# Kernel optimization log

Measured on AMD Instinct MI355X. Metric: run time of the kernel, lower is better.

Reference implementation:

```python
import jax, jax.numpy as jnp
import numpy as np

H = 8        # n_heads (== n_kv_heads)
D = 128      # head_dim
WINDOW = 16  # sliding window (left); causal => right window = 0
EPS = 1e-6   # qk_norm_eps


def rms_norm(x, w, eps=EPS):
    # RMSNorm over last dim with learnable scale
    ms = jnp.mean(jnp.square(x), axis=-1, keepdims=True)
    return x * jax.lax.rsqrt(ms + eps) * w


def setup_inputs() -> dict:
    key = jax.random.key(0)
    ks = jax.random.split(key, 5)
    B, S, dim = 4, 2048, 1024
    scale = 1.0 / np.sqrt(dim)
    return {
        "x": jax.random.normal(ks[0], (B, S, dim), jnp.float32),
        "wq": jax.random.normal(ks[1], (dim, dim), jnp.float32) * scale,
        "wk": jax.random.normal(ks[2], (dim, dim), jnp.float32) * scale,
        "wv": jax.random.normal(ks[3], (dim, dim), jnp.float32) * scale,
        "wo": jax.random.normal(ks[4], (dim, dim), jnp.float32) * scale,
        "q_norm_w": jnp.ones((dim,), jnp.float32),
        "k_norm_w": jnp.ones((dim,), jnp.float32),
    }


def reference(x, wq, wk, wv, wo, q_norm_w, k_norm_w):
    B, S, dim = x.shape
    # projections (torch Linear: x @ W.T)
    xq = rms_norm(x @ wq.T, q_norm_w)
    xk = rms_norm(x @ wk.T, k_norm_w)
    xv = x @ wv.T
    q = xq.reshape(B, S, H, D)
    k = xk.reshape(B, S, H, D)
    v = xv.reshape(B, S, H, D)

    # ALiBi slopes for 8 heads (power of two): 2^-1 .. 2^-8
    slopes = jnp.exp2(-jnp.arange(1, H + 1, dtype=jnp.float32))
    pos = jnp.arange(S)
    rel = pos[None, :] - pos[:, None]          # [S, S], rel[i, j] = j - i
    bias = slopes[:, None, None] * rel.astype(x.dtype)   # [H, S, S]
    masked = (rel > 0) | (rel < -WINDOW)       # causal + sliding window
    bias = jnp.where(masked[None], -jnp.inf, bias)

    scores = jnp.einsum('bqhd,bkhd->bhqk', q, k) / np.sqrt(D) + bias[None]
    attn = jax.nn.softmax(scores, axis=-1)
    out = jnp.einsum('bhqk,bkhd->bqhd', attn, v).reshape(B, S, H * D)
    return out @ wo.T
```

## Files before the change

### kernel.cpp

```cpp
#include <hip/hip_runtime.h>
#include <math.h>

#define NHEADS 8
#define HDIM   128
#define WIN    16
#define DIM    1024
#define QKVDIM 3072
#define SEQ    2048
#define BATCH  4
#define MROWS  (BATCH * SEQ)
#define RMS_EPS 1e-6f
#define PLANE  ((size_t)MROWS * HDIM)

typedef __bf16 bf16x8 __attribute__((ext_vector_type(8)));
typedef unsigned short u16x8 __attribute__((ext_vector_type(8)));
typedef float  f32x4  __attribute__((ext_vector_type(4)));

__device__ __forceinline__ unsigned short f2b(float f) {
    union { float f; unsigned u; } c; c.f = f;
    return (unsigned short)((c.u + 0x7FFFu + ((c.u >> 16) & 1u)) >> 16);
}
__device__ __forceinline__ float b2f(unsigned short u) {
    union { unsigned u; float f; } c; c.u = ((unsigned)u) << 16; return c.f;
}
__device__ __forceinline__ bf16x8 u2b(u16x8 u) {
    union { u16x8 u; bf16x8 b; } c; c.u = u; return c.b;
}

__device__ __forceinline__ void storec(unsigned short* p, float v) { *p = f2b(v); }
__device__ __forceinline__ void storec(float* p, float v) { *p = v; }

__global__ __launch_bounds__(256) void cast_all(const float* __restrict__ x,
                                                const float* __restrict__ w0,
                                                const float* __restrict__ w1,
                                                const float* __restrict__ w2,
                                                const float* __restrict__ w3,
                                                unsigned short* __restrict__ xb,
                                                unsigned short* __restrict__ wb,
                                                float* __restrict__ sumsq)
{
    const int b = blockIdx.x;
    const int t = threadIdx.x;
    if (b >= 12288) {
        ((float4*)sumsq)[(b - 12288) * 256 + t] = make_float4(0.f, 0.f, 0.f, 0.f);
        return;
    }
    const float* src;
    unsigned short* dst;
    int i;
    if (b < 8192) {
        i = b * 256 + t;
        src = x; dst = xb;
    } else {
        const int bb = b - 8192;
        const int which = bb >> 10;
        i = (bb & 1023) * 256 + t;
        src = which == 0 ? w0 : which == 1 ? w1 : which == 2 ? w2 : w3;
        dst = wb + (size_t)which * DIM * DIM;
    }
    const float4 v = ((const float4*)src)[i];
    ushort4 o;
    o.x = f2b(v.x); o.y = f2b(v.y); o.z = f2b(v.z); o.w = f2b(v.w);
    ((ushort4*)dst)[i] = o;
}

#define BARR do { asm volatile("s_barrier" ::: "memory"); __builtin_amdgcn_sched_barrier(0); } while (0)
#define WAITV(N) asm volatile("s_waitcnt vmcnt(" #N ")" ::: "memory")

#define LDA8(mh, b) { \
    _Pragma("unroll") for (int il = 0; il < 4; ++il) { \
        const int rr = (wm * 128 + (mh) * 64 + il * 16 + frow) * 64; \
        af[il][0] = *(const bf16x8*)&As[b][rr + cs0]; \
        af[il][1] = *(const bf16x8*)&As[b][rr + cs1]; \
    } }

#define LDB4(nh, b, bgr) { \
    _Pragma("unroll") for (int jl = 0; jl < 2; ++jl) { \
        const int rr = (wn * 64 + (nh) * 32 + jl * 16 + frow) * 64; \
        bgr[jl][0] = *(const bf16x8*)&Bs[b][rr + cs0]; \
        bgr[jl][1] = *(const bf16x8*)&Bs[b][rr + cs1]; \
    } }

#define MMA16(mh, nh, bgr) { \
    __builtin_amdgcn_s_setprio(1); \
    _Pragma("unroll") for (int il = 0; il < 4; ++il) \
    _Pragma("unroll") for (int jl = 0; jl < 2; ++jl) { \
        acc[(mh)*4+il][(nh)*2+jl] = __builtin_amdgcn_mfma_f32_16x16x32_bf16(af[il][0], bgr[jl][0], acc[(mh)*4+il][(nh)*2+jl], 0, 0, 0); \
        acc[(mh)*4+il][(nh)*2+jl] = __builtin_amdgcn_mfma_f32_16x16x32_bf16(af[il][1], bgr[jl][1], acc[(mh)*4+il][(nh)*2+jl], 0, 0, 0); \
    } \
    __builtin_amdgcn_s_setprio(0); }

#define STAGE_A(b, half, kt) { \
    _Pragma("unroll") for (int s2 = 0; s2 < 2; ++s2) { \
        const int rb = (half) * 128 + s2 * 64; \
        __builtin_amdgcn_global_load_lds( \
            (const __attribute__((address_space(1))) void*)(gA + (size_t)rb * K + (kt)), \
            (__attribute__((address_space(3))) void*)&As[b][(rb + wid * 8) * 64], 16, 0, 0); \
    } }

#define STAGE_B(b, half, kt) { \
    _Pragma("unroll") for (int s2 = 0; s2 < 2; ++s2) { \
        const int rb = (half) * 128 + s2 * 64; \
        __builtin_amdgcn_global_load_lds( \
            (const __attribute__((address_space(1))) void*)(gB + (size_t)rb * K + (kt)), \
            (__attribute__((address_space(3))) void*)&Bs[b][(rb + wid * 8) * 64], 16, 0, 0); \
    } }

__global__ __launch_bounds__(512, 2) void gemm_nt_256(const unsigned short* __restrict__ A,
                                                      const unsigned short* __restrict__ B,
                                                      unsigned short* __restrict__ Cq,
                                                      float* __restrict__ sumsq,
                                                      int M, int N, int K)
{
    __shared__ __align__(16) __bf16 As[2][256 * 64];
    __shared__ __align__(16) __bf16 Bs[2][256 * 64];

    const int t    = threadIdx.x;
    const int wid  = t >> 6;
    const int lane = t & 63;
    const int wm   = wid >> 2;
    const int wn   = wid & 3;
    const int bm0  = blockIdx.y * 256;
    const int bn0  = blockIdx.x * 256;

    const int frow = lane & 15;
    const int quad = lane >> 4;
    const int cs0  = ((quad    ) ^ (frow & 7)) * 8;
    const int cs1  = ((quad + 4) ^ (frow & 7)) * 8;

    const int lr = lane >> 3;
    const int lc = (lane & 7) ^ lr;
    const unsigned short* gA = A + (size_t)(bm0 + wid * 8 + lr) * K + lc * 8;
    const unsigned short* gB = B + (size_t)(bn0 + wid * 8 + lr) * K + lc * 8;

    f32x4 acc[8][4];
    #pragma unroll
    for (int i = 0; i < 8; ++i)
        #pragma unroll
        for (int j = 0; j < 4; ++j)
            #pragma unroll
            for (int e = 0; e < 4; ++e) acc[i][j][e] = 0.f;

    bf16x8 af[4][2], bg0[2][2], bg1[2][2];

    const int NI = K >> 7;

    STAGE_B(0, 0, 0); STAGE_B(0, 1, 0); STAGE_A(0, 0, 0); STAGE_A(0, 1, 0);
    STAGE_B(1, 0, 64); STAGE_B(1, 1, 64);
    WAITV(4);
    BARR;

    for (int i = 0; i < NI; ++i) {
        const bool last = (i == NI - 1);
        const int kt0 = i << 7;
        LDA8(0, 0); LDB4(0, 0, bg0);
        STAGE_A(1, 0, kt0 + 64);
        BARR; MMA16(0, 0, bg0); BARR;
        LDB4(1, 0, bg1);
        STAGE_A(1, 1, kt0 + 64);
        BARR; MMA16(0, 1, bg1); BARR;
        LDA8(1, 0);
        if (!last) STAGE_B(0, 0, kt0 + 128);
        BARR; MMA16(1, 1, bg1); BARR;
        if (!last) STAGE_B(0, 1, kt0 + 128);
        BARR; MMA16(1, 0, bg0);
        if (last) { WAITV(0); } else { WAITV(4); }
        BARR;
        LDA8(0, 1); LDB4(0, 1, bg0);
        if (!last) STAGE_A(0, 0, kt0 + 128);
        BARR; MMA16(0, 0, bg0); BARR;
        LDB4(1, 1, bg1);
        if (!last) STAGE_A(0, 1, kt0 + 128);
        BARR; MMA16(0, 1, bg1); BARR;
        LDA8(1, 1);
        if (!last) STAGE_B(1, 0, kt0 + 192);
        BARR; MMA16(1, 1, bg1); BARR;
        if (!last) STAGE_B(1, 1, kt0 + 192);
        BARR; MMA16(1, 0, bg0);
        if (!last) { WAITV(4); }
        BARR;
    }

    const int m_base = bm0 + wm * 128;
    const int n_base = bn0 + wn * 64;
    size_t cb[4];
    #pragma unroll
    for (int j = 0; j < 4; ++j) {
        const int nb = n_base + j * 16;
        cb[j] = (size_t)(nb >> 7) * PLANE + (nb & 127);
    }
    #pragma unroll
    for (int i2 = 0; i2 < 8; ++i2)
        #pragma unroll
        for (int r = 0; r < 4; ++r) {
            const size_t row = m_base + i2 * 16 + quad * 4 + r;
            #pragma unroll
            for (int j = 0; j < 4; ++j)
                Cq[cb[j] + row * HDIM + frow] = f2b(acc[i2][j][r]);
        }

    if (sumsq != nullptr && bn0 < 2 * DIM) {
        const int which = bn0 >> 10;
        #pragma unroll
        for (int i2 = 0; i2 < 8; ++i2)
            #pragma unroll
            for (int r = 0; r < 4; ++r) {
                float p = acc[i2][0][r] * acc[i2][0][r] + acc[i2][1][r] * acc[i2][1][r]
                        + acc[i2][2][r] * acc[i2][2][r] + acc[i2][3][r] * acc[i2][3][r];
                p += __shfl_xor(p, 1, 64);
                p += __shfl_xor(p, 2, 64);
                p += __shfl_xor(p, 4, 64);
                p += __shfl_xor(p, 8, 64);
                if (frow == 0)
                    atomicAdd(&sumsq[(size_t)(m_base + i2 * 16 + quad * 4 + r) * 2 + which], p);
            }
    }
}

template <typename TC>
__global__ __launch_bounds__(256) void gemm_nt_mfma(const unsigned short* __restrict__ A,
                                                    const unsigned short* __restrict__ B,
                                                    TC* __restrict__ C,
                                                    int M, int N, int K)
{
    __shared__ __align__(16) __bf16 As[128 * 64];
    __shared__ __align__(16) __bf16 Bs[128 * 64];

    const int t    = threadIdx.x;
    const int w    = t >> 6;
    const int lane = t & 63;
    const int wm   = w >> 1;
    const int wn   = w & 1;
    const int bm0  = blockIdx.y * 128;
    const int bn0  = blockIdx.x * 128;

    const int lrow   = lane >> 3;
    const int lchunk = (lane & 7) ^ (lrow & 7);
    const size_t laneoff = (size_t)lrow * K + lchunk * 8;

    const unsigned short* gA = A + (size_t)bm0 * K + laneoff;
    const unsigned short* gB = B + (size_t)bn0 * K + laneoff;

    const int frow = lane & 15;
    const int quad = lane >> 4;
    const int cs0 = ((quad    ) ^ (frow & 7)) * 8;
    const int cs1 = ((quad + 4) ^ (frow & 7)) * 8;

    f32x4 acc[4][4];
    #pragma unroll
    for (int i = 0; i < 4; ++i)
        #pragma unroll
        for (int j = 0; j < 4; ++j)
            #pragma unroll
            for (int e = 0; e < 4; ++e) acc[i][j][e] = 0.f;

    for (int kt = 0; kt < K; kt += 64) {
        __syncthreads();
        #pragma unroll
        for (int s = 0; s < 4; ++s) {
            const int seg = w * 4 + s;
            __builtin_amdgcn_global_load_lds(
                (const __attribute__((address_space(1))) void*)(gA + (size_t)seg * 8 * K + kt),
                (__attribute__((address_space(3))) void*)&As[seg * 512], 16, 0, 0);
            __builtin_amdgcn_global_load_lds(
                (const __attribute__((address_space(1))) void*)(gB + (size_t)seg * 8 * K + kt),
                (__attribute__((address_space(3))) void*)&Bs[seg * 512], 16, 0, 0);
        }
        __syncthreads();

        #pragma unroll
        for (int sub = 0; sub < 2; ++sub) {
            const int cs = sub ? cs1 : cs0;
            bf16x8 af[4], bg[4];
            #pragma unroll
            for (int i = 0; i < 4; ++i) {
                af[i] = *(const bf16x8*)&As[(wm * 64 + i * 16 + frow) * 64 + cs];
                bg[i] = *(const bf16x8*)&Bs[(wn * 64 + i * 16 + frow) * 64 + cs];
            }
            #pragma unroll
            for (int i = 0; i < 4; ++i)
                #pragma unroll
                for (int j = 0; j < 4; ++j)
                    acc[i][j] = __builtin_amdgcn_mfma_f32_16x16x32_bf16(af[i], bg[j], acc[i][j], 0, 0, 0);
        }
    }

    const int m_base = bm0 + wm * 64;
    const int n_base = bn0 + wn * 64;
    const int col    = frow;
    const int rquad  = quad * 4;
    #pragma unroll
    for (int i = 0; i < 4; ++i)
        #pragma unroll
        for (int r = 0; r < 4; ++r) {
            TC* crow = C + (size_t)(m_base + i * 16 + rquad + r) * N + n_base + col;
            #pragma unroll
            for (int j = 0; j < 4; ++j)
                storec(crow + j * 16, acc[i][j][r]);
        }
}

__global__ __launch_bounds__(256) void attn_mfma(const unsigned short* __restrict__ qkvp,
                                                 const float* __restrict__ sumsq,
                                                 const float* __restrict__ qw,
                                                 const float* __restrict__ kw,
                                                 unsigned short* __restrict__ o)
{
    __shared__ __align__(16) unsigned short Vt[128 * 88];
    __shared__ __align__(16) unsigned short Plds[4 * 16 * 40];

    const int t  = threadIdx.x;
    const int qb = blockIdx.x;
    const int h  = blockIdx.y;
    const int r0 = qb * 64;
    const int i0 = r0 & (SEQ - 1);
    const int bb = r0 - i0;

    const unsigned short* qg = qkvp + (size_t)h * PLANE;
    const unsigned short* kg = qkvp + (size_t)(NHEADS + h) * PLANE;
    const unsigned short* vg = qkvp + (size_t)(2 * NHEADS + h) * PLANE;

    #pragma unroll
    for (int it = 0; it < 5; ++it) {
        const int c = it * 256 + t;
        const int c8 = c / 80, lr2 = c - c8 * 80;
        const int ks = i0 - 16 + lr2;
        const int rc = ks < 0 ? 0 : ks;
        const u16x8 vv = *(const u16x8*)(vg + (size_t)(bb + rc) * HDIM + c8 * 8);
        #pragma unroll
        for (int e = 0; e < 8; ++e)
            Vt[(c8 * 8 + e) * 88 + lr2] = vv[e];
    }

    const int w    = t >> 6;
    const int lane = t & 63;
    const int frow = lane & 15;
    const int quad = lane >> 4;
    const int fk   = quad * 8;

    const size_t qrow = (size_t)(r0 + w * 16 + frow) * HDIM;
    const int kidx0   = i0 - 16 + w * 16 + frow;
    const int kr0     = kidx0 < 0 ? 0 : kidx0;
    const size_t krow0 = (size_t)(bb + kr0) * HDIM;
    const size_t krow1 = (size_t)(r0 + w * 16 + frow) * HDIM;

    f32x4 s0 = {0.f, 0.f, 0.f, 0.f}, s1 = {0.f, 0.f, 0.f, 0.f};
    #pragma unroll
    for (int kt = 0; kt < 4; ++kt) {
        const u16x8 qa = *(const u16x8*)(qg + qrow + kt * 32 + fk);
        u16x8 qn;
        #pragma unroll
        for (int e = 0; e < 8; ++e) {
            const int d = h * HDIM + kt * 32 + fk + e;
            qn[e] = f2b(b2f(qa[e]) * qw[d] * kw[d]);
        }
        const bf16x8 af = u2b(qn);
        const bf16x8 b0 = *(const bf16x8*)(kg + krow0 + kt * 32 + fk);
        const bf16x8 b1 = *(const bf16x8*)(kg + krow1 + kt * 32 + fk);
        s0 = __builtin_amdgcn_mfma_f32_16x16x32_bf16(af, b0, s0, 0, 0, 0);
        s1 = __builtin_amdgcn_mfma_f32_16x16x32_bf16(af, b1, s1, 0, 0, 0);
    }

    const float ksc0 = rsqrtf(sumsq[(size_t)(bb + kr0) * 2 + 1] * (1.0f / DIM) + RMS_EPS);
    const float ksc1 = rsqrtf(sumsq[(size_t)(r0 + w * 16 + frow) * 2 + 1] * (1.0f / DIM) + RMS_EPS);
    float qs[4];
    #pragma unroll
    for (int r = 0; r < 4; ++r)
        qs[r] = rsqrtf(sumsq[(size_t)(r0 + w * 16 + quad * 4 + r) * 2] * (1.0f / DIM) + RMS_EPS);

    const float scl   = 0.088388347648318447f;
    const float slope = exp2f(-(float)(h + 1));
    const bool  lead  = (i0 == 0) && (w == 0);
    const int   col   = frow;
    float inv[4];
    #pragma unroll
    for (int r = 0; r < 4; ++r) {
        const int m = quad * 4 + r;
        const float sc0 = scl * qs[r] * ksc0;
        const float sc1 = scl * qs[r] * ksc1;
        float v0 = (col < m || lead) ? -1e30f : s0[r] * sc0 + slope * (float)(col - 16 - m);
        float v1 = (col > m)         ? -1e30f : s1[r] * sc1 + slope * (float)(col - m);
        float mx = fmaxf(v0, v1);
        #pragma unroll
        for (int off = 1; off < 16; off <<= 1) mx = fmaxf(mx, __shfl_xor(mx, off, 64));
        const float e0 = __expf(v0 - mx);
        const float e1 = __expf(v1 - mx);
        float sm = e0 + e1;
        #pragma unroll
        for (int off = 1; off < 16; off <<= 1) sm += __shfl_xor(sm, off, 64);
        inv[r] = 1.0f / sm;
        Plds[(w * 16 + m) * 40 + col]      = f2b(e0);
        Plds[(w * 16 + m) * 40 + 16 + col] = f2b(e1);
    }

    __syncthreads();

    const bf16x8 pf = *(const bf16x8*)&Plds[(w * 16 + frow) * 40 + fk];
    f32x4 oa[8];
    #pragma unroll
    for (int nt = 0; nt < 8; ++nt) {
        oa[nt][0] = 0.f; oa[nt][1] = 0.f; oa[nt][2] = 0.f; oa[nt][3] = 0.f;
        const bf16x8 vf = *(const bf16x8*)&Vt[(nt * 16 + frow) * 88 + w * 16 + fk];
        oa[nt] = __builtin_amdgcn_mfma_f32_16x16x32_bf16(pf, vf, oa[nt], 0, 0, 0);
    }

    #pragma unroll
    for (int nt = 0; nt < 8; ++nt)
        #pragma unroll
        for (int r = 0; r < 4; ++r) {
            const int m = quad * 4 + r;
            o[(size_t)(r0 + w * 16 + m) * DIM + h * HDIM + nt * 16 + col] =
                f2b(oa[nt][r] * inv[r]);
        }
}

extern "C" void kernel_launch(void* const* d_in, const int* in_sizes, int n_in,
                              void* d_out, int out_size, void* d_ws, size_t ws_size,
                              hipStream_t stream)
{
    const float* x  = (const float*)d_in[0];
    const float* wq = (const float*)d_in[1];
    const float* wk = (const float*)d_in[2];
    const float* wv = (const float*)d_in[3];
    const float* wo = (const float*)d_in[4];
    const float* qw = (const float*)d_in[5];
    const float* kw = (const float*)d_in[6];
    float* out = (float*)d_out;

    unsigned short* xb   = (unsigned short*)d_ws;
    unsigned short* wb   = xb + (size_t)MROWS * DIM;
    unsigned short* qkvp = wb + (size_t)4 * DIM * DIM;
    unsigned short* ob   = qkvp + (size_t)MROWS * QKVDIM;
    float*          ssq  = (float*)(ob + (size_t)MROWS * DIM);
    unsigned short* wob  = wb + (size_t)3 * DIM * DIM;

    cast_all<<<12304, 256, 0, stream>>>(x, wq, wk, wv, wo, xb, wb, ssq);

    gemm_nt_256<<<dim3(QKVDIM / 256, MROWS / 256), 512, 0, stream>>>(
        xb, wb, qkvp, ssq, MROWS, QKVDIM, DIM);

    attn_mfma<<<dim3(MROWS / 64, NHEADS), 256, 0, stream>>>(qkvp, ssq, qw, kw, ob);

    gemm_nt_mfma<float><<<dim3(DIM / 128, MROWS / 128), 256, 0, stream>>>(
        ob, wob, out, MROWS, DIM, DIM);
}
```

Before: 222.8 us.

## Unify GEMMs into 256x128-tile double-buffered kernel for QKV and output projections

Result: faster. 215.7 us (-3.2%).

```diff
diff --git a/kernel.cpp b/kernel.cpp
--- a/kernel.cpp
+++ b/kernel.cpp
@@ -26,9 +26,6 @@
 __device__ __forceinline__ bf16x8 u2b(u16x8 u) {
     union { u16x8 u; bf16x8 b; } c; c.u = u; return c.b;
 }
-
-__device__ __forceinline__ void storec(unsigned short* p, float v) { *p = f2b(v); }
-__device__ __forceinline__ void storec(float* p, float v) { *p = v; }
 
 __global__ __launch_bounds__(256) void cast_all(const float* __restrict__ x,
                                                 const float* __restrict__ w0,
@@ -67,61 +64,62 @@
 #define BARR do { asm volatile("s_barrier" ::: "memory"); __builtin_amdgcn_sched_barrier(0); } while (0)
 #define WAITV(N) asm volatile("s_waitcnt vmcnt(" #N ")" ::: "memory")
 
-#define LDA8(mh, b) { \
+#define LDA8(b) { \
     _Pragma("unroll") for (int il = 0; il < 4; ++il) { \
-        const int rr = (wm * 128 + (mh) * 64 + il * 16 + frow) * 64; \
+        const int rr = (wm * 64 + il * 16 + frow) * 64; \
         af[il][0] = *(const bf16x8*)&As[b][rr + cs0]; \
         af[il][1] = *(const bf16x8*)&As[b][rr + cs1]; \
     } }
 
-#define LDB4(nh, b, bgr) { \
+#define LDB4(bh, b, bgr) { \
     _Pragma("unroll") for (int jl = 0; jl < 2; ++jl) { \
-        const int rr = (wn * 64 + (nh) * 32 + jl * 16 + frow) * 64; \
+        const int rr = (wn * 64 + (bh) * 32 + jl * 16 + frow) * 64; \
         bgr[jl][0] = *(const bf16x8*)&Bs[b][rr + cs0]; \
         bgr[jl][1] = *(const bf16x8*)&Bs[b][rr + cs1]; \
     } }
 
-#define MMA16(mh, nh, bgr) { \
+#define MMA16(bh, bgr) { \
     __builtin_amdgcn_s_setprio(1); \
     _Pragma("unroll") for (int il = 0; il < 4; ++il) \
     _Pragma("unroll") for (int jl = 0; jl < 2; ++jl) { \
-        acc[(mh)*4+il][(nh)*2+jl] = __builtin_amdgcn_mfma_f32_16x16x32_bf16(af[il][0], bgr[jl][0], acc[(mh)*4+il][(nh)*2+jl], 0, 0, 0); \
-        acc[(mh)*4+il][(nh)*2+jl] = __builtin_amdgcn_mfma_f32_16x16x32_bf16(af[il][1], bgr[jl][1], acc[(mh)*4+il][(nh)*2+jl], 0, 0, 0); \
+        acc[il][(bh)*2+jl] = __builtin_amdgcn_mfma_f32_16x16x32_bf16(af[il][0], bgr[jl][0], acc[il][(bh)*2+jl], 0, 0, 0); \
+        acc[il][(bh)*2+jl] = __builtin_amdgcn_mfma_f32_16x16x32_bf16(af[il][1], bgr[jl][1], acc[il][(bh)*2+jl], 0, 0, 0); \
     } \
     __builtin_amdgcn_s_setprio(0); }
 
-#define STAGE_A(b, half, kt) { \
-    _Pragma("unroll") for (int s2 = 0; s2 < 2; ++s2) { \
-        const int rb = (half) * 128 + s2 * 64; \
+#define STAGE_A(b, kt) { \
+    _Pragma("unroll") for (int s2 = 0; s2 < 4; ++s2) { \
+        const int rb = s2 * 64; \
         __builtin_amdgcn_global_load_lds( \
             (const __attribute__((address_space(1))) void*)(gA + (size_t)rb * K + (kt)), \
             (__attribute__((address_space(3))) void*)&As[b][(rb + wid * 8) * 64], 16, 0, 0); \
     } }
 
-#define STAGE_B(b, half, kt) { \
+#define STAGE_B(b, kt) { \
     _Pragma("unroll") for (int s2 = 0; s2 < 2; ++s2) { \
-        const int rb = (half) * 128 + s2 * 64; \
+        const int rb = s2 * 64; \
         __builtin_amdgcn_global_load_lds( \
             (const __attribute__((address_space(1))) void*)(gB + (size_t)rb * K + (kt)), \
             (__attribute__((address_space(3))) void*)&Bs[b][(rb + wid * 8) * 64], 16, 0, 0); \
     } }
 
-__global__ __launch_bounds__(512, 2) void gemm_nt_256(const unsigned short* __restrict__ A,
-                                                      const unsigned short* __restrict__ B,
-                                                      unsigned short* __restrict__ Cq,
-                                                      float* __restrict__ sumsq,
-                                                      int M, int N, int K)
+template <typename TC, bool PLANAR>
+__global__ __launch_bounds__(512, 2) void gemm_nt_bm256(const unsigned short* __restrict__ A,
+                                                        const unsigned short* __restrict__ B,
+                                                        TC* __restrict__ C,
+                                                        float* __restrict__ sumsq,
+                                                        int M, int N, int K)
 {
     __shared__ __align__(16) __bf16 As[2][256 * 64];
-    __shared__ __align__(16) __bf16 Bs[2][256 * 64];
+    __shared__ __align__(16) __bf16 Bs[2][128 * 64];
 
     const int t    = threadIdx.x;
     const int wid  = t >> 6;
     const int lane = t & 63;
-    const int wm   = wid >> 2;
-    const int wn   = wid & 3;
+    const int wm   = wid >> 1;
+    const int wn   = wid & 1;
     const int bm0  = blockIdx.y * 256;
-    const int bn0  = blockIdx.x * 256;
+    const int bn0  = blockIdx.x * 128;
 
     const int frow = lane & 15;
     const int quad = lane >> 4;
@@ -133,9 +131,9 @@
     const unsigned short* gA = A + (size_t)(bm0 + wid * 8 + lr) * K + lc * 8;
     const unsigned short* gB = B + (size_t)(bn0 + wid * 8 + lr) * K + lc * 8;
 
-    f32x4 acc[8][4];
-    #pragma unroll
-    for (int i = 0; i < 8; ++i)
+    f32x4 acc[4][4];
+    #pragma unroll
+    for (int i = 0; i < 4; ++i)
         #pragma unroll
         for (int j = 0; j < 4; ++j)
             #pragma unroll
@@ -143,161 +141,71 @@
 
     bf16x8 af[4][2], bg0[2][2], bg1[2][2];
 
-    const int NI = K >> 7;
-
-    STAGE_B(0, 0, 0); STAGE_B(0, 1, 0); STAGE_A(0, 0, 0); STAGE_A(0, 1, 0);
-    STAGE_B(1, 0, 64); STAGE_B(1, 1, 64);
-    WAITV(4);
+    const int NI = K >> 6;
+
+    STAGE_B(0, 0); STAGE_A(0, 0); STAGE_B(1, 64);
+    WAITV(2);
     BARR;
 
     for (int i = 0; i < NI; ++i) {
-        const bool last = (i == NI - 1);
-        const int kt0 = i << 7;
-        LDA8(0, 0); LDB4(0, 0, bg0);
-        STAGE_A(1, 0, kt0 + 64);
-        BARR; MMA16(0, 0, bg0); BARR;
-        LDB4(1, 0, bg1);
-        STAGE_A(1, 1, kt0 + 64);
-        BARR; MMA16(0, 1, bg1); BARR;
-        LDA8(1, 0);
-        if (!last) STAGE_B(0, 0, kt0 + 128);
-        BARR; MMA16(1, 1, bg1); BARR;
-        if (!last) STAGE_B(0, 1, kt0 + 128);
-        BARR; MMA16(1, 0, bg0);
-        if (last) { WAITV(0); } else { WAITV(4); }
+        const int cur = i & 1;
+        const int nxt = cur ^ 1;
+        const int kt  = i << 6;
+        LDA8(cur); LDB4(0, cur, bg0); LDB4(1, cur, bg1);
+        if (i + 1 < NI) STAGE_A(nxt, kt + 64);
+        BARR; MMA16(0, bg0); BARR;
+        if (i + 2 < NI) STAGE_B(cur, kt + 128);
+        BARR; MMA16(1, bg1);
+        if (i + 2 < NI)      { WAITV(2); }
+        else if (i + 1 < NI) { WAITV(0); }
         BARR;
-        LDA8(0, 1); LDB4(0, 1, bg0);
-        if (!last) STAGE_A(0, 0, kt0 + 128);
-        BARR; MMA16(0, 0, bg0); BARR;
-        LDB4(1, 1, bg1);
-        if (!last) STAGE_A(0, 1, kt0 + 128);
-        BARR; MMA16(0, 1, bg1); BARR;
-        LDA8(1, 1);
-        if (!last) STAGE_B(1, 0, kt0 + 192);
-        BARR; MMA16(1, 1, bg1); BARR;
-        if (!last) STAGE_B(1, 1, kt0 + 192);
-        BARR; MMA16(1, 0, bg0);
-        if (!last) { WAITV(4); }
-        BARR;
-    }
-
-    const int m_base = bm0 + wm * 128;
+    }
+
+    const int m_base = bm0 + wm * 64;
     const int n_base = bn0 + wn * 64;
-    size_t cb[4];
-    #pragma unroll
-    for (int j = 0; j < 4; ++j) {
-        const int nb = n_base + j * 16;
-        cb[j] = (size_t)(nb >> 7) * PLANE + (nb & 127);
-    }
-    #pragma unroll
-    for (int i2 = 0; i2 < 8; ++i2)
-        #pragma unroll
-        for (int r = 0; r < 4; ++r) {
-            const size_t row = m_base + i2 * 16 + quad * 4 + r;
-            #pragma unroll
-            for (int j = 0; j < 4; ++j)
-                Cq[cb[j] + row * HDIM + frow] = f2b(acc[i2][j][r]);
+    if constexpr (PLANAR) {
+        size_t cb[4];
+        #pragma unroll
+        for (int j = 0; j < 4; ++j) {
+            const int nb = n_base + j * 16;
+            cb[j] = (size_t)(nb >> 7) * PLANE + (nb & 127);
         }
-
-    if (sumsq != nullptr && bn0 < 2 * DIM) {
-        const int which = bn0 >> 10;
-        #pragma unroll
-        for (int i2 = 0; i2 < 8; ++i2)
+        #pragma unroll
+        for (int il = 0; il < 4; ++il)
             #pragma unroll
             for (int r = 0; r < 4; ++r) {
-                float p = acc[i2][0][r] * acc[i2][0][r] + acc[i2][1][r] * acc[i2][1][r]
-                        + acc[i2][2][r] * acc[i2][2][r] + acc[i2][3][r] * acc[i2][3][r];
-                p += __shfl_xor(p, 1, 64);
-                p += __shfl_xor(p, 2, 64);
-                p += __shfl_xor(p, 4, 64);
-                p += __shfl_xor(p, 8, 64);
-                if (frow == 0)
-                    atomicAdd(&sumsq[(size_t)(m_base + i2 * 16 + quad * 4 + r) * 2 + which], p);
-            }
-    }
-}
-
-template <typename TC>
-__global__ __launch_bounds__(256) void gemm_nt_mfma(const unsigned short* __restrict__ A,
-                                                    const unsigned short* __restrict__ B,
-                                                    TC* __restrict__ C,
-                                                    int M, int N, int K)
-{
-    __shared__ __align__(16) __bf16 As[128 * 64];
-    __shared__ __align__(16) __bf16 Bs[128 * 64];
-
-    const int t    = threadIdx.x;
-    const int w    = t >> 6;
-    const int lane = t & 63;
-    const int wm   = w >> 1;
-    const int wn   = w & 1;
-    const int bm0  = blockIdx.y * 128;
-    const int bn0  = blockIdx.x * 128;
-
-    const int lrow   = lane >> 3;
-    const int lchunk = (lane & 7) ^ (lrow & 7);
-    const size_t laneoff = (size_t)lrow * K + lchunk * 8;
-
-    const unsigned short* gA = A + (size_t)bm0 * K + laneoff;
-    const unsigned short* gB = B + (size_t)bn0 * K + laneoff;
-
-    const int frow = lane & 15;
-    const int quad = lane >> 4;
-    const int cs0 = ((quad    ) ^ (frow & 7)) * 8;
-    const int cs1 = ((quad + 4) ^ (frow & 7)) * 8;
-
-    f32x4 acc[4][4];
-    #pragma unroll
-    for (int i = 0; i < 4; ++i)
-        #pragma unroll
-        for (int j = 0; j < 4; ++j)
-            #pragma unroll
-            for (int e = 0; e < 4; ++e) acc[i][j][e] = 0.f;
-
-    for (int kt = 0; kt < K; kt += 64) {
-        __syncthreads();
-        #pragma unroll
-        for (int s = 0; s < 4; ++s) {
-            const int seg = w * 4 + s;
-            __builtin_amdgcn_global_load_lds(
-                (const __attribute__((address_space(1))) void*)(gA + (size_t)seg * 8 * K + kt),
-                (__attribute__((address_space(3))) void*)&As[seg * 512], 16, 0, 0);
-            __builtin_amdgcn_global_load_lds(
-                (const __attribute__((address_space(1))) void*)(gB + (size_t)seg * 8 * K + kt),
-                (__attribute__((address_space(3))) void*)&Bs[seg * 512], 16, 0, 0);
-        }
-        __syncthreads();
-
-        #pragma unroll
-        for (int sub = 0; sub < 2; ++sub) {
-            const int cs = sub ? cs1 : cs0;
-            bf16x8 af[4], bg[4];
-            #pragma unroll
-            for (int i = 0; i < 4; ++i) {
-                af[i] = *(const bf16x8*)&As[(wm * 64 + i * 16 + frow) * 64 + cs];
-                bg[i] = *(const bf16x8*)&Bs[(wn * 64 + i * 16 + frow) * 64 + cs];
-            }
-            #pragma unroll
-            for (int i = 0; i < 4; ++i)
+                const size_t row = m_base + il * 16 + quad * 4 + r;
                 #pragma unroll
                 for (int j = 0; j < 4; ++j)
-                    acc[i][j] = __builtin_amdgcn_mfma_f32_16x16x32_bf16(af[i], bg[j], acc[i][j], 0, 0, 0);
+                    ((unsigned short*)C)[cb[j] + row * HDIM + frow] = f2b(acc[il][j][r]);
+            }
+        if (sumsq != nullptr && bn0 < 2 * DIM) {
+            const int which = bn0 >> 10;
+            #pragma unroll
+            for (int il = 0; il < 4; ++il)
+                #pragma unroll
+                for (int r = 0; r < 4; ++r) {
+                    float p = acc[il][0][r] * acc[il][0][r] + acc[il][1][r] * acc[il][1][r]
+                            + acc[il][2][r] * acc[il][2][r] + acc[il][3][r] * acc[il][3][r];
+                    p += __shfl_xor(p, 1, 64);
+                    p += __shfl_xor(p, 2, 64);
+                    p += __shfl_xor(p, 4, 64);
+                    p += __shfl_xor(p, 8, 64);
+                    if (frow == 0)
+                        atomicAdd(&sumsq[(size_t)(m_base + il * 16 + quad * 4 + r) * 2 + which], p);
+                }
         }
-    }
-
-    const int m_base = bm0 + wm * 64;
-    const int n_base = bn0 + wn * 64;
-    const int col    = frow;
-    const int rquad  = quad * 4;
-    #pragma unroll
-    for (int i = 0; i < 4; ++i)
-        #pragma unroll
-        for (int r = 0; r < 4; ++r) {
-            TC* crow = C + (size_t)(m_base + i * 16 + rquad + r) * N + n_base + col;
+    } else {
+        #pragma unroll
+        for (int il = 0; il < 4; ++il)
             #pragma unroll
-            for (int j = 0; j < 4; ++j)
-                storec(crow + j * 16, acc[i][j][r]);
-        }
+            for (int r = 0; r < 4; ++r) {
+                TC* crow = C + (size_t)(m_base + il * 16 + quad * 4 + r) * N + n_base + frow;
+                #pragma unroll
+                for (int j = 0; j < 4; ++j)
+                    crow[j * 16] = acc[il][j][r];
+            }
+    }
 }
 
 __global__ __launch_bounds__(256) void attn_mfma(const unsigned short* __restrict__ qkvp,
@@ -436,11 +344,11 @@
 
     cast_all<<<12304, 256, 0, stream>>>(x, wq, wk, wv, wo, xb, wb, ssq);
 
-    gemm_nt_256<<<dim3(QKVDIM / 256, MROWS / 256), 512, 0, stream>>>(
+    gemm_nt_bm256<unsigned short, true><<<dim3(QKVDIM / 128, MROWS / 256), 512, 0, stream>>>(
         xb, wb, qkvp, ssq, MROWS, QKVDIM, DIM);
 
     attn_mfma<<<dim3(MROWS / 64, NHEADS), 256, 0, stream>>>(qkvp, ssq, qw, kw, ob);
 
-    gemm_nt_mfma<float><<<dim3(DIM / 128, MROWS / 128), 256, 0, stream>>>(
-        ob, wob, out, MROWS, DIM, DIM);
-}
+    gemm_nt_bm256<float, false><<<dim3(DIM / 128, MROWS / 256), 512, 0, stream>>>(
+        ob, wob, out, nullptr, MROWS, DIM, DIM);
+}
```
